# Kernel optimization log

Hardware: AMD Instinct MI355X
Metric: run time of the kernel (lower is better)

The kernel has to match this reference:

```python
import jax, jax.numpy as jnp
import numpy as np

H = 256   # rnn_hidden_size
E = 300   # embedding_size
B = 64    # batch
S = 64    # french seq len
T = 32    # max_en_length (decode steps)
VF = 32000  # french vocab
VE = 32000  # english vocab
BOS = 1


def gru_cell(x, h, wih, whh, bih, bhh):
    # torch GRUCell math: r,z,n gates, weights stored as [3H, in]/[3H, H]
    gi = x @ wih.T + bih
    gh = h @ whh.T + bhh
    ir, iz, inn = jnp.split(gi, 3, axis=-1)
    hr, hz, hn = jnp.split(gh, 3, axis=-1)
    r = jax.nn.sigmoid(ir + hr)
    z = jax.nn.sigmoid(iz + hz)
    n = jnp.tanh(inn + r * hn)
    return (1.0 - z) * n + z * h


def run_gru_dir(xs, wih, whh, bih, bhh, reverse):
    # xs: (B, S, F) -> final hidden (B, H), outputs (B, S, H) in original time order
    h0 = jnp.zeros((xs.shape[0], H), xs.dtype)
    def step(h, x):
        h2 = gru_cell(x, h, wih, whh, bih, bhh)
        return h2, h2
    hT, ys = jax.lax.scan(step, h0, jnp.swapaxes(xs, 0, 1), reverse=reverse)
    return hT, jnp.swapaxes(ys, 0, 1)


def setup_inputs() -> dict:
    key = jax.random.key(0)
    ks = iter(jax.random.split(key, 64))
    def n(shape, s=0.05):
        return jax.random.normal(next(ks), shape, dtype=jnp.float32) * s
    d = {}
    d["fr"] = jax.random.randint(next(ks), (B, S), 0, VF)
    d["fr_emb"] = n((VF, E), 0.3)
    d["en_emb"] = n((VE, E), 0.3)
    # encoder: 2 layers, bidirectional; leading dim 2 = (fwd, bwd)
    d["enc0_wih"] = n((2, 3 * H, E));      d["enc0_whh"] = n((2, 3 * H, H))
    d["enc0_bih"] = n((2, 3 * H));         d["enc0_bhh"] = n((2, 3 * H))
    d["enc1_wih"] = n((2, 3 * H, 2 * H));  d["enc1_whh"] = n((2, 3 * H, H))
    d["enc1_bih"] = n((2, 3 * H));         d["enc1_bhh"] = n((2, 3 * H))
    # decoder: 2 layers, unidirectional
    d["dec0_wih"] = n((3 * H, E));  d["dec0_whh"] = n((3 * H, H))
    d["dec0_bih"] = n((3 * H,));   d["dec0_bhh"] = n((3 * H,))
    d["dec1_wih"] = n((3 * H, H)); d["dec1_whh"] = n((3 * H, H))
    d["dec1_bih"] = n((3 * H,));   d["dec1_bhh"] = n((3 * H,))
    d["hid_w"] = n((H, 2 * H));   d["hid_b"] = n((H,))      # hidden_transformer
    d["encT_w"] = n((H, 2 * H));  d["encT_b"] = n((H,))     # encoding_transformer
    d["attn_w"] = n((H, H));      d["attn_b"] = n((H,))     # attention.hidden_linear
    d["tot_w"] = n((1, H));       d["tot_b"] = n((1,))      # attention.total_linear
    d["rnnT_w"] = n((E, 2 * H + E)); d["rnnT_b"] = n((E,))  # rnn_transformer
    d["voc_w"] = n((VE, H));      d["voc_b"] = n((VE,))     # to_vocab
    return d


def _forward(fr, fr_emb, en_emb,
             enc0_wih, enc0_whh, enc0_bih, enc0_bhh,
             enc1_wih, enc1_whh, enc1_bih, enc1_bhh,
             dec0_wih, dec0_whh, dec0_bih, dec0_bhh,
             dec1_wih, dec1_whh, dec1_bih, dec1_bhh,
             hid_w, hid_b, encT_w, encT_b, attn_w, attn_b,
             tot_w, tot_b, rnnT_w, rnnT_b, voc_w, voc_b):
    bsz = fr.shape[0]
    x = fr_emb[fr]  # (B,S,E)
    hs = []
    for (wih, whh, bih, bhh) in ((enc0_wih, enc0_whh, enc0_bih, enc0_bhh),
                                 (enc1_wih, enc1_whh, enc1_bih, enc1_bhh)):
        hf, yf = run_gru_dir(x, wih[0], whh[0], bih[0], bhh[0], reverse=False)
        hb, yb = run_gru_dir(x, wih[1], whh[1], bih[1], bhh[1], reverse=True)
        x = jnp.concatenate([yf, yb], axis=-1)  # (B,S,2H)
        hs += [hf, hb]
    encoding = x  # (B,S,2H)
    hidden = jnp.stack(hs)                       # (4,B,H) torch layout [l0f,l0b,l1f,l1b]
    hidden = hidden.reshape(2, bsz, 2 * H)       # faithful to torch .view (row-major)
    hidden = hidden @ hid_w.T + hid_b            # (2,B,H)
    trans_enc = encoding @ encT_w.T + encT_b     # (B,S,H)
    seq = en_emb[jnp.full((bsz, 1), BOS, dtype=jnp.int32)]  # (B,1,E); dropout in eval

    def dec_step(carry, _):
        hidden, seq = carry
        hq = hidden[-1][:, None, :]  # (B,1,H)
        a = jnp.tanh(trans_enc + hq @ attn_w.T + attn_b)        # (B,S,H)
        attn = jax.nn.softmax(a @ tot_w.T + tot_b, axis=1)      # (B,S,1)
        weighted = jnp.sum(attn * encoding, axis=1, keepdims=True)  # (B,1,2H)
        seq2 = jnp.concatenate([weighted, seq], axis=-1) @ rnnT_w.T + rnnT_b  # (B,1,E)
        xt = seq2[:, 0]
        h0 = gru_cell(xt, hidden[0], dec0_wih, dec0_whh, dec0_bih, dec0_bhh)
        h1 = gru_cell(h0, hidden[1], dec1_wih, dec1_whh, dec1_bih, dec1_bhh)
        logits = h1 @ voc_w.T + voc_b  # (B,VE)
        tok = jnp.argmax(logits, axis=-1)
        new_seq = en_emb[tok][:, None, :]
        return (jnp.stack([h0, h1]), new_seq), logits

    _, logits = jax.lax.scan(dec_step, (hidden, seq), None, length=T)
    return jnp.transpose(logits, (1, 0, 2))  # (B,T,VE)


def reference(fr, fr_emb, en_emb,
              enc0_wih, enc0_whh, enc0_bih, enc0_bhh,
              enc1_wih, enc1_whh, enc1_bih, enc1_bhh,
              dec0_wih, dec0_whh, dec0_bih, dec0_bhh,
              dec1_wih, dec1_whh, dec1_bih, dec1_bhh,
              hid_w, hid_b, encT_w, encT_b, attn_w, attn_b,
              tot_w, tot_b, rnnT_w, rnnT_b, voc_w, voc_b):
    return _forward(fr, fr_emb, en_emb,
                    enc0_wih, enc0_whh, enc0_bih, enc0_bhh,
                    enc1_wih, enc1_whh, enc1_bih, enc1_bhh,
                    dec0_wih, dec0_whh, dec0_bih, dec0_bhh,
                    dec1_wih, dec1_whh, dec1_bih, dec1_bhh,
                    hid_w, hid_b, encT_w, encT_b, attn_w, attn_b,
                    tot_w, tot_b, rnnT_w, rnnT_b, voc_w, voc_b)
```

## Files before the change

### kernel.cpp

```cpp
#include <hip/hip_runtime.h>
#include <math.h>

#define HD 256
#define ED 300
#define BD 64
#define SD 64
#define TD 32
#define VD 32000

__global__ void k_transpose(const float* __restrict__ in, float* __restrict__ out, int R, int K) {
    int i = blockIdx.x * 256 + threadIdx.x;
    if (i < R * K) {
        int r = i / K, k = i - r * K;
        out[(size_t)k * R + r] = in[i];
    }
}

__global__ void k_emb(const int* __restrict__ fr, const float* __restrict__ emb, float* __restrict__ x) {
    int i = blockIdx.x * 256 + threadIdx.x;
    if (i < 4096 * 300) {
        int m = i / 300, k = i - m * 300;
        int s = m >> 6, b = m & 63;
        int tok = fr[b * 64 + s];
        x[i] = emb[(size_t)tok * 300 + k];
    }
}

__launch_bounds__(256)
__global__ void k_gemm(const float* __restrict__ A, const float* __restrict__ B,
                       const float* __restrict__ bias, float* __restrict__ C,
                       int M, int N, int K) {
    __shared__ float As[16][68];
    __shared__ float Bs[16][68];
    int tid = threadIdx.x;
    int m0 = blockIdx.x * 64;
    int n0 = blockIdx.y * 64;
    int tx = tid & 15, ty = tid >> 4;
    float acc[4][4] = {};
    for (int k0 = 0; k0 < K; k0 += 16) {
        for (int e = tid; e < 1024; e += 256) {
            int mm = e >> 4, kk = e & 15;
            int k = k0 + kk;
            As[kk][mm] = (k < K) ? A[(size_t)(m0 + mm) * K + k] : 0.f;
        }
        for (int e = tid; e < 1024; e += 256) {
            int nn = e >> 4, kk = e & 15;
            int k = k0 + kk;
            Bs[kk][nn] = (k < K) ? B[(size_t)(n0 + nn) * K + k] : 0.f;
        }
        __syncthreads();
#pragma unroll
        for (int kk = 0; kk < 16; ++kk) {
            float4 a4 = *(const float4*)&As[kk][ty * 4];
            float4 b4 = *(const float4*)&Bs[kk][tx * 4];
            float av[4] = {a4.x, a4.y, a4.z, a4.w};
            float bv[4] = {b4.x, b4.y, b4.z, b4.w};
#pragma unroll
            for (int i = 0; i < 4; ++i)
#pragma unroll
                for (int j = 0; j < 4; ++j)
                    acc[i][j] += av[i] * bv[j];
        }
        __syncthreads();
    }
#pragma unroll
    for (int i = 0; i < 4; ++i) {
        int m = m0 + ty * 4 + i;
#pragma unroll
        for (int j = 0; j < 4; ++j) {
            int n = n0 + tx * 4 + j;
            C[(size_t)m * N + n] = acc[i][j] + (bias ? bias[n] : 0.f);
        }
    }
}

__launch_bounds__(512)
__global__ void k_rec(const float* __restrict__ gi, const float* __restrict__ whh_t,
                      const float* __restrict__ bhh, float* __restrict__ ys,
                      float* __restrict__ hfin) {
    __shared__ float h[2][256];
    __shared__ float part[2][3][256];
    int tid = threadIdx.x;
    int d = blockIdx.x >> 5;
    int b0 = (blockIdx.x & 31) * 2;
    h[tid >> 8][tid & 255] = 0.f;
    __syncthreads();
    int lb = 0, g = 0, qj = 0;
    bool qact = tid < 384;
    if (qact) { lb = tid / 192; int q = tid % 192; g = q >> 6; qj = q & 63; }
    const float* wp = whh_t + (size_t)d * 768 + g * 256 + qj * 4;

    for (int step = 0; step < 64; ++step) {
        int s = d ? (63 - step) : step;
        if (qact) {
            float a0 = 0.f, a1 = 0.f, a2 = 0.f, a3 = 0.f;
            const float* hp = h[lb];
#pragma unroll 4
            for (int k = 0; k < 256; ++k) {
                float4 w4 = *(const float4*)(wp + (size_t)k * 1536);
                float hk = hp[k];
                a0 += w4.x * hk; a1 += w4.y * hk; a2 += w4.z * hk; a3 += w4.w * hk;
            }
            part[lb][g][qj * 4 + 0] = a0;
            part[lb][g][qj * 4 + 1] = a1;
            part[lb][g][qj * 4 + 2] = a2;
            part[lb][g][qj * 4 + 3] = a3;
        }
        __syncthreads();
        {
            int plb = tid >> 8, j = tid & 255;
            int b = b0 + plb;
            const float* gib = gi + (size_t)(s * 64 + b) * 1536 + d * 768;
            float gr = part[plb][0][j] + bhh[d * 768 + j];
            float gz = part[plb][1][j] + bhh[d * 768 + 256 + j];
            float gn = part[plb][2][j] + bhh[d * 768 + 512 + j];
            float r = 1.f / (1.f + expf(-(gib[j] + gr)));
            float z = 1.f / (1.f + expf(-(gib[256 + j] + gz)));
            float n = tanhf(gib[512 + j] + r * gn);
            float hv = h[plb][j];
            float hn = (1.f - z) * n + z * hv;
            ys[(size_t)(s * 64 + b) * 512 + d * 256 + j] = hn;
            if (step == 63) hfin[(size_t)(d * 64 + b) * 256 + j] = hn;
            h[plb][j] = hn;
        }
        __syncthreads();
    }
}

__global__ void k_hpack(const float* __restrict__ hf0, const float* __restrict__ hf1,
                        float* __restrict__ A) {
    int i = blockIdx.x * 256 + threadIdx.x;
    if (i < 128 * 512) {
        int m = i >> 9, c = i & 511;
        int l = m >> 6, b2 = m & 63;
        int d = b2 >> 5;
        int b = 2 * (b2 & 31) + (c >> 8);
        int hh = c & 255;
        const float* src = l ? hf1 : hf0;
        A[i] = src[(size_t)(d * 64 + b) * 256 + hh];
    }
}

__launch_bounds__(256)
__global__ void k_dec1(int t,
                       const float* __restrict__ pval, const int* __restrict__ pidx,
                       const float* __restrict__ en_emb,
                       const float* __restrict__ attn_w, const float* __restrict__ attn_b,
                       const float* __restrict__ tot_w, const float* __restrict__ tot_b,
                       const float* __restrict__ te, const float* __restrict__ enc,
                       const float* __restrict__ rnnT_w, const float* __restrict__ rnnT_b,
                       const float* __restrict__ d0_wih, const float* __restrict__ d0_whh,
                       const float* __restrict__ d0_bih, const float* __restrict__ d0_bhh,
                       const float* __restrict__ d1_wih, const float* __restrict__ d1_whh,
                       const float* __restrict__ d1_bih, const float* __restrict__ d1_bhh,
                       float* __restrict__ hdec) {
    int b = blockIdx.x;
    int tid = threadIdx.x;
    __shared__ float seqv[304];
    __shared__ float hq[256];
    __shared__ float h0[256];
    __shared__ float aq[256];
    __shared__ float scred[64][4];
    __shared__ float sc[64];
    __shared__ float attnv[64];
    __shared__ float wsum[512];
    __shared__ float xt[304];
    __shared__ float h0n[256];
    __shared__ int tok_s;

    if (t == 0) {
        if (tid == 0) tok_s = 1;
    } else if (tid < 64) {
        float v = -INFINITY; int idx = 0x7fffffff;
        if (tid < 63) { v = pval[b * 64 + tid]; idx = pidx[b * 64 + tid]; }
        for (int off = 32; off > 0; off >>= 1) {
            float v2 = __shfl_down(v, off);
            int i2 = __shfl_down(idx, off);
            if (v2 > v || (v2 == v && i2 < idx)) { v = v2; idx = i2; }
        }
        if (tid == 0) tok_s = idx;
    }
    __syncthreads();
    int tok = tok_s;
    for (int e = tid; e < 300; e += 256) seqv[e] = en_emb[(size_t)tok * 300 + e];
    hq[tid] = hdec[(size_t)(64 + b) * 256 + tid];
    h0[tid] = hdec[(size_t)b * 256 + tid];
    __syncthreads();

    {
        float acc = attn_b[tid];
        const float* wr = attn_w + (size_t)tid * 256;
#pragma unroll 4
        for (int k = 0; k < 256; k += 4) {
            float4 w4 = *(const float4*)(wr + k);
            float4 h4 = *(const float4*)&hq[k];
            acc += w4.x * h4.x + w4.y * h4.y + w4.z * h4.z + w4.w * h4.w;
        }
        aq[tid] = acc;
    }
    __syncthreads();

    {
        int s = tid >> 2, p = tid & 3;
        const float* tep = te + (size_t)(s * 64 + b) * 256 + p * 64;
        float acc = 0.f;
        for (int jj = 0; jj < 64; ++jj)
            acc += tot_w[p * 64 + jj] * tanhf(tep[jj] + aq[p * 64 + jj]);
        scred[s][p] = acc;
    }
    __syncthreads();
    if (tid < 64) sc[tid] = scred[tid][0] + scred[tid][1] + scred[tid][2] + scred[tid][3] + tot_b[0];
    __syncthreads();

    if (tid < 64) {
        float v = sc[tid];
        float m = v;
        for (int off = 32; off > 0; off >>= 1) m = fmaxf(m, __shfl_xor(m, off));
        float e = expf(v - m);
        float sum = e;
        for (int off = 32; off > 0; off >>= 1) sum += __shfl_xor(sum, off);
        attnv[tid] = e / sum;
    }
    __syncthreads();

    for (int c = tid; c < 512; c += 256) {
        float acc = 0.f;
        for (int s = 0; s < 64; ++s) acc += attnv[s] * enc[(size_t)(s * 64 + b) * 512 + c];
        wsum[c] = acc;
    }
    __syncthreads();

    for (int e = tid; e < 300; e += 256) {
        float acc = rnnT_b[e];
        const float* wr = rnnT_w + (size_t)e * 812;
#pragma unroll 4
        for (int c = 0; c < 512; c += 4) {
            float4 w4 = *(const float4*)(wr + c);
            float4 s4 = *(const float4*)&wsum[c];
            acc += w4.x * s4.x + w4.y * s4.y + w4.z * s4.z + w4.w * s4.w;
        }
#pragma unroll 4
        for (int c = 0; c < 300; c += 4) {
            float4 w4 = *(const float4*)(wr + 512 + c);
            float4 s4 = *(const float4*)&seqv[c];
            acc += w4.x * s4.x + w4.y * s4.y + w4.z * s4.z + w4.w * s4.w;
        }
        xt[e] = acc;
    }
    __syncthreads();

    {
        int j = tid;
        float g0 = d0_bih[j], g1 = d0_bih[256 + j], g2 = d0_bih[512 + j];
#pragma unroll 2
        for (int k = 0; k < 300; k += 4) {
            float4 x4 = *(const float4*)&xt[k];
            float4 wa = *(const float4*)&d0_wih[(size_t)j * 300 + k];
            float4 wb = *(const float4*)&d0_wih[(size_t)(256 + j) * 300 + k];
            float4 wc = *(const float4*)&d0_wih[(size_t)(512 + j) * 300 + k];
            g0 += wa.x * x4.x + wa.y * x4.y + wa.z * x4.z + wa.w * x4.w;
            g1 += wb.x * x4.x + wb.y * x4.y + wb.z * x4.z + wb.w * x4.w;
            g2 += wc.x * x4.x + wc.y * x4.y + wc.z * x4.z + wc.w * x4.w;
        }
        float r0 = d0_bhh[j], r1 = d0_bhh[256 + j], r2 = d0_bhh[512 + j];
#pragma unroll 2
        for (int k = 0; k < 256; k += 4) {
            float4 h4 = *(const float4*)&h0[k];
            float4 wa = *(const float4*)&d0_whh[(size_t)j * 256 + k];
            float4 wb = *(const float4*)&d0_whh[(size_t)(256 + j) * 256 + k];
            float4 wc = *(const float4*)&d0_whh[(size_t)(512 + j) * 256 + k];
            r0 += wa.x * h4.x + wa.y * h4.y + wa.z * h4.z + wa.w * h4.w;
            r1 += wb.x * h4.x + wb.y * h4.y + wb.z * h4.z + wb.w * h4.w;
            r2 += wc.x * h4.x + wc.y * h4.y + wc.z * h4.z + wc.w * h4.w;
        }
        float r = 1.f / (1.f + expf(-(g0 + r0)));
        float z = 1.f / (1.f + expf(-(g1 + r1)));
        float n = tanhf(g2 + r * r2);
        float hnv = (1.f - z) * n + z * h0[j];
        hdec[(size_t)b * 256 + j] = hnv;
        h0n[j] = hnv;
    }
    __syncthreads();

    {
        int j = tid;
        float g0 = d1_bih[j], g1 = d1_bih[256 + j], g2 = d1_bih[512 + j];
#pragma unroll 2
        for (int k = 0; k < 256; k += 4) {
            float4 x4 = *(const float4*)&h0n[k];
            float4 wa = *(const float4*)&d1_wih[(size_t)j * 256 + k];
            float4 wb = *(const float4*)&d1_wih[(size_t)(256 + j) * 256 + k];
            float4 wc = *(const float4*)&d1_wih[(size_t)(512 + j) * 256 + k];
            g0 += wa.x * x4.x + wa.y * x4.y + wa.z * x4.z + wa.w * x4.w;
            g1 += wb.x * x4.x + wb.y * x4.y + wb.z * x4.z + wb.w * x4.w;
            g2 += wc.x * x4.x + wc.y * x4.y + wc.z * x4.z + wc.w * x4.w;
        }
        float r0 = d1_bhh[j], r1 = d1_bhh[256 + j], r2 = d1_bhh[512 + j];
#pragma unroll 2
        for (int k = 0; k < 256; k += 4) {
            float4 h4 = *(const float4*)&hq[k];
            float4 wa = *(const float4*)&d1_whh[(size_t)j * 256 + k];
            float4 wb = *(const float4*)&d1_whh[(size_t)(256 + j) * 256 + k];
            float4 wc = *(const float4*)&d1_whh[(size_t)(512 + j) * 256 + k];
            r0 += wa.x * h4.x + wa.y * h4.y + wa.z * h4.z + wa.w * h4.w;
            r1 += wb.x * h4.x + wb.y * h4.y + wb.z * h4.z + wb.w * h4.w;
            r2 += wc.x * h4.x + wc.y * h4.y + wc.z * h4.z + wc.w * h4.w;
        }
        float r = 1.f / (1.f + expf(-(g0 + r0)));
        float z = 1.f / (1.f + expf(-(g1 + r1)));
        float n = tanhf(g2 + r * r2);
        float hnv = (1.f - z) * n + z * hq[j];
        hdec[(size_t)(64 + b) * 256 + j] = hnv;
    }
}

__launch_bounds__(256)
__global__ void k_dec2(int t, const float* __restrict__ voc_w, const float* __restrict__ voc_b,
                       const float* __restrict__ hdec, float* __restrict__ out,
                       float* __restrict__ pval, int* __restrict__ pidx) {
    int vb = blockIdx.x, bc = blockIdx.y;
    int tid = threadIdx.x;
    int v0 = vb * 512;
    int b0 = bc * 8;
    __shared__ float hl[8][256];
    __shared__ float rv[256];
    __shared__ int ri[256];
    for (int e = tid; e < 2048; e += 256) {
        int bb = e >> 8, k = e & 255;
        hl[bb][k] = hdec[(size_t)(64 + b0 + bb) * 256 + k];
    }
    __syncthreads();
    int v1 = v0 + tid;
    int v2 = v0 + 256 + tid;
    bool has2 = v2 < VD;
    float acc1[8], acc2[8];
    float b1v = voc_b[v1];
    float b2v = has2 ? voc_b[v2] : 0.f;
#pragma unroll
    for (int bb = 0; bb < 8; ++bb) { acc1[bb] = b1v; acc2[bb] = b2v; }
    for (int k = 0; k < 256; k += 4) {
        float4 w1 = *(const float4*)&voc_w[(size_t)v1 * 256 + k];
        float4 w2 = make_float4(0.f, 0.f, 0.f, 0.f);
        if (has2) w2 = *(const float4*)&voc_w[(size_t)v2 * 256 + k];
#pragma unroll
        for (int bb = 0; bb < 8; ++bb) {
            float4 h4 = *(const float4*)&hl[bb][k];
            acc1[bb] += w1.x * h4.x + w1.y * h4.y + w1.z * h4.z + w1.w * h4.w;
            acc2[bb] += w2.x * h4.x + w2.y * h4.y + w2.z * h4.z + w2.w * h4.w;
        }
    }
    for (int bb = 0; bb < 8; ++bb) {
        int b = b0 + bb;
        out[((size_t)b * 32 + t) * VD + v1] = acc1[bb];
        if (has2) out[((size_t)b * 32 + t) * VD + v2] = acc2[bb];
        float bv = acc1[bb]; int bi = v1;
        if (has2 && (acc2[bb] > bv)) { bv = acc2[bb]; bi = v2; }
        rv[tid] = bv; ri[tid] = bi;
        __syncthreads();
        for (int stn = 128; stn > 0; stn >>= 1) {
            if (tid < stn) {
                float ov = rv[tid + stn]; int oi = ri[tid + stn];
                if (ov > rv[tid] || (ov == rv[tid] && oi < ri[tid])) { rv[tid] = ov; ri[tid] = oi; }
            }
            __syncthreads();
        }
        if (tid == 0) { pval[(size_t)b * 64 + vb] = rv[0]; pidx[(size_t)b * 64 + vb] = ri[0]; }
        __syncthreads();
    }
}

extern "C" void kernel_launch(void* const* d_in, const int* in_sizes, int n_in,
                              void* d_out, int out_size, void* d_ws, size_t ws_size,
                              hipStream_t stream) {
    (void)in_sizes; (void)n_in; (void)out_size; (void)ws_size;
    const int*   fr     = (const int*)  d_in[0];
    const float* fr_emb = (const float*)d_in[1];
    const float* en_emb = (const float*)d_in[2];
    const float* e0_wih = (const float*)d_in[3];
    const float* e0_whh = (const float*)d_in[4];
    const float* e0_bih = (const float*)d_in[5];
    const float* e0_bhh = (const float*)d_in[6];
    const float* e1_wih = (const float*)d_in[7];
    const float* e1_whh = (const float*)d_in[8];
    const float* e1_bih = (const float*)d_in[9];
    const float* e1_bhh = (const float*)d_in[10];
    const float* d0_wih = (const float*)d_in[11];
    const float* d0_whh = (const float*)d_in[12];
    const float* d0_bih = (const float*)d_in[13];
    const float* d0_bhh = (const float*)d_in[14];
    const float* d1_wih = (const float*)d_in[15];
    const float* d1_whh = (const float*)d_in[16];
    const float* d1_bih = (const float*)d_in[17];
    const float* d1_bhh = (const float*)d_in[18];
    const float* hid_w  = (const float*)d_in[19];
    const float* hid_b  = (const float*)d_in[20];
    const float* encT_w = (const float*)d_in[21];
    const float* encT_b = (const float*)d_in[22];
    const float* attn_w = (const float*)d_in[23];
    const float* attn_b = (const float*)d_in[24];
    const float* tot_w  = (const float*)d_in[25];
    const float* tot_b  = (const float*)d_in[26];
    const float* rnnT_w = (const float*)d_in[27];
    const float* rnnT_b = (const float*)d_in[28];
    const float* voc_w  = (const float*)d_in[29];
    const float* voc_b  = (const float*)d_in[30];
    float* out = (float*)d_out;

    float* ws = (float*)d_ws;
    size_t o = 0;
    auto take = [&](size_t n) { size_t r = o; o += (n + 15) & ~(size_t)15; return r; };
    float* whh0t = ws + take(256 * 1536);
    float* whh1t = ws + take(256 * 1536);
    float* xbuf  = ws + take((size_t)4096 * 300);
    float* gi    = ws + take((size_t)4096 * 1536);
    float* ys0   = ws + take((size_t)4096 * 512);
    float* ys1   = ws + take((size_t)4096 * 512);
    float* te    = ws + take((size_t)4096 * 256);
    float* hfin0 = ws + take(2 * 64 * 256);
    float* hfin1 = ws + take(2 * 64 * 256);
    float* ahid  = ws + take(128 * 512);
    float* hdec  = ws + take(128 * 256);
    float* pval  = ws + take(64 * 64);
    int*   pidx  = (int*)(ws + take(64 * 64));

    k_transpose<<<(1536 * 256 + 255) / 256, 256, 0, stream>>>(e0_whh, whh0t, 1536, 256);
    k_transpose<<<(1536 * 256 + 255) / 256, 256, 0, stream>>>(e1_whh, whh1t, 1536, 256);
    k_emb<<<(4096 * 300 + 255) / 256, 256, 0, stream>>>(fr, fr_emb, xbuf);
    k_gemm<<<dim3(64, 24), 256, 0, stream>>>(xbuf, e0_wih, e0_bih, gi, 4096, 1536, 300);
    k_rec<<<64, 512, 0, stream>>>(gi, whh0t, e0_bhh, ys0, hfin0);
    k_gemm<<<dim3(64, 24), 256, 0, stream>>>(ys0, e1_wih, e1_bih, gi, 4096, 1536, 512);
    k_rec<<<64, 512, 0, stream>>>(gi, whh1t, e1_bhh, ys1, hfin1);
    k_gemm<<<dim3(64, 4), 256, 0, stream>>>(ys1, encT_w, encT_b, te, 4096, 256, 512);
    k_hpack<<<256, 256, 0, stream>>>(hfin0, hfin1, ahid);
    k_gemm<<<dim3(2, 4), 256, 0, stream>>>(ahid, hid_w, hid_b, hdec, 128, 256, 512);
    for (int t = 0; t < 32; ++t) {
        k_dec1<<<64, 256, 0, stream>>>(t, pval, pidx, en_emb, attn_w, attn_b, tot_w, tot_b,
                                       te, ys1, rnnT_w, rnnT_b,
                                       d0_wih, d0_whh, d0_bih, d0_bhh,
                                       d1_wih, d1_whh, d1_bih, d1_bhh, hdec);
        k_dec2<<<dim3(63, 8), 256, 0, stream>>>(t, voc_w, voc_b, hdec, out, pval, pidx);
    }
}
```

Measured before the change: 12.62 ms.

## Rework GEMM tiling, recurrence, decoder and vocab projection kernels

Replaces the 64x64 GEMM with a 128x128 tile using 8x8 per-thread accumulators and float4 loads. Rewrites the encoder recurrence as one block per (direction, batch), with each thread reading its own rows of whh, which removes the transpose kernels. Widens the decoder step kernel to 1024 threads, splitting its dot products across threads with shuffle reductions. Restructures the vocab projection into 1000 blocks of 32 vocab rows covering all batches, with a transposed output staging buffer and more partial argmax entries. Workspace buffers are aliased to cut memory use, which adds reuse-ordering risk, and the larger GEMM tiles launch fewer blocks.

Result: faster. 10.94 ms (-13.3%).

```diff
diff --git a/kernel.cpp b/kernel.cpp
--- a/kernel.cpp
+++ b/kernel.cpp
@@ -1,19 +1,10 @@
 #include <hip/hip_runtime.h>
 #include <math.h>
 
-#define HD 256
-#define ED 300
-#define BD 64
-#define SD 64
-#define TD 32
 #define VD 32000
 
-__global__ void k_transpose(const float* __restrict__ in, float* __restrict__ out, int R, int K) {
-    int i = blockIdx.x * 256 + threadIdx.x;
-    if (i < R * K) {
-        int r = i / K, k = i - r * K;
-        out[(size_t)k * R + r] = in[i];
-    }
+__device__ __forceinline__ float dot4f(float4 a, float4 b) {
+    return a.x*b.x + a.y*b.y + a.z*b.z + a.w*b.w;
 }
 
 __global__ void k_emb(const int* __restrict__ fr, const float* __restrict__ emb, float* __restrict__ x) {
@@ -27,102 +18,102 @@
 }
 
 __launch_bounds__(256)
-__global__ void k_gemm(const float* __restrict__ A, const float* __restrict__ B,
-                       const float* __restrict__ bias, float* __restrict__ C,
-                       int M, int N, int K) {
-    __shared__ float As[16][68];
-    __shared__ float Bs[16][68];
+__global__ void k_gemm128(const float* __restrict__ A, const float* __restrict__ B,
+                          const float* __restrict__ bias, float* __restrict__ C,
+                          int M, int N, int K) {
+    __shared__ __align__(16) float As[16][132];
+    __shared__ __align__(16) float Bs[16][132];
     int tid = threadIdx.x;
-    int m0 = blockIdx.x * 64;
-    int n0 = blockIdx.y * 64;
+    int m0 = blockIdx.x * 128;
+    int n0 = blockIdx.y * 128;
     int tx = tid & 15, ty = tid >> 4;
-    float acc[4][4] = {};
+    float acc[8][8] = {};
     for (int k0 = 0; k0 < K; k0 += 16) {
-        for (int e = tid; e < 1024; e += 256) {
-            int mm = e >> 4, kk = e & 15;
-            int k = k0 + kk;
-            As[kk][mm] = (k < K) ? A[(size_t)(m0 + mm) * K + k] : 0.f;
-        }
-        for (int e = tid; e < 1024; e += 256) {
-            int nn = e >> 4, kk = e & 15;
-            int k = k0 + kk;
-            Bs[kk][nn] = (k < K) ? B[(size_t)(n0 + nn) * K + k] : 0.f;
+#pragma unroll
+        for (int l = 0; l < 2; ++l) {
+            int e = tid + l * 256;
+            int row = e >> 2, kc = (e & 3) << 2;
+            int k = k0 + kc;
+            float4 va = make_float4(0.f, 0.f, 0.f, 0.f);
+            float4 vb = make_float4(0.f, 0.f, 0.f, 0.f);
+            if (k < K) {
+                va = *(const float4*)&A[(size_t)(m0 + row) * K + k];
+                vb = *(const float4*)&B[(size_t)(n0 + row) * K + k];
+            }
+            As[kc + 0][row] = va.x; As[kc + 1][row] = va.y; As[kc + 2][row] = va.z; As[kc + 3][row] = va.w;
+            Bs[kc + 0][row] = vb.x; Bs[kc + 1][row] = vb.y; Bs[kc + 2][row] = vb.z; Bs[kc + 3][row] = vb.w;
         }
         __syncthreads();
 #pragma unroll
         for (int kk = 0; kk < 16; ++kk) {
-            float4 a4 = *(const float4*)&As[kk][ty * 4];
-            float4 b4 = *(const float4*)&Bs[kk][tx * 4];
-            float av[4] = {a4.x, a4.y, a4.z, a4.w};
-            float bv[4] = {b4.x, b4.y, b4.z, b4.w};
-#pragma unroll
-            for (int i = 0; i < 4; ++i)
-#pragma unroll
-                for (int j = 0; j < 4; ++j)
-                    acc[i][j] += av[i] * bv[j];
+            float a[8], bb[8];
+            *(float4*)&a[0]  = *(const float4*)&As[kk][ty * 8];
+            *(float4*)&a[4]  = *(const float4*)&As[kk][ty * 8 + 4];
+            *(float4*)&bb[0] = *(const float4*)&Bs[kk][tx * 8];
+            *(float4*)&bb[4] = *(const float4*)&Bs[kk][tx * 8 + 4];
+#pragma unroll
+            for (int i = 0; i < 8; ++i)
+#pragma unroll
+                for (int j = 0; j < 8; ++j)
+                    acc[i][j] += a[i] * bb[j];
         }
         __syncthreads();
     }
 #pragma unroll
-    for (int i = 0; i < 4; ++i) {
-        int m = m0 + ty * 4 + i;
-#pragma unroll
-        for (int j = 0; j < 4; ++j) {
-            int n = n0 + tx * 4 + j;
-            C[(size_t)m * N + n] = acc[i][j] + (bias ? bias[n] : 0.f);
-        }
-    }
-}
-
-__launch_bounds__(512)
-__global__ void k_rec(const float* __restrict__ gi, const float* __restrict__ whh_t,
+    for (int i = 0; i < 8; ++i) {
+        int m = m0 + ty * 8 + i;
+#pragma unroll
+        for (int j = 0; j < 8; j += 4) {
+            int n = n0 + tx * 8 + j;
+            float4 o;
+            o.x = acc[i][j + 0] + (bias ? bias[n + 0] : 0.f);
+            o.y = acc[i][j + 1] + (bias ? bias[n + 1] : 0.f);
+            o.z = acc[i][j + 2] + (bias ? bias[n + 2] : 0.f);
+            o.w = acc[i][j + 3] + (bias ? bias[n + 3] : 0.f);
+            *(float4*)&C[(size_t)m * N + n] = o;
+        }
+    }
+}
+
+__launch_bounds__(256)
+__global__ void k_rec(const float* __restrict__ gi, const float* __restrict__ whh,
                       const float* __restrict__ bhh, float* __restrict__ ys,
                       float* __restrict__ hfin) {
-    __shared__ float h[2][256];
-    __shared__ float part[2][3][256];
-    int tid = threadIdx.x;
-    int d = blockIdx.x >> 5;
-    int b0 = (blockIdx.x & 31) * 2;
-    h[tid >> 8][tid & 255] = 0.f;
-    __syncthreads();
-    int lb = 0, g = 0, qj = 0;
-    bool qact = tid < 384;
-    if (qact) { lb = tid / 192; int q = tid % 192; g = q >> 6; qj = q & 63; }
-    const float* wp = whh_t + (size_t)d * 768 + g * 256 + qj * 4;
-
+    __shared__ __align__(16) float h[256];
+    int u = threadIdx.x;
+    int d = blockIdx.x >> 6;
+    int b = blockIdx.x & 63;
+    h[u] = 0.f;
+    const float* wr_ = whh + ((size_t)d * 768 + u) * 256;
+    const float* wz_ = wr_ + 256 * 256;
+    const float* wn_ = wr_ + 512 * 256;
+    float br = bhh[d * 768 + u];
+    float bz = bhh[d * 768 + 256 + u];
+    float bn = bhh[d * 768 + 512 + u];
+    __syncthreads();
     for (int step = 0; step < 64; ++step) {
         int s = d ? (63 - step) : step;
-        if (qact) {
-            float a0 = 0.f, a1 = 0.f, a2 = 0.f, a3 = 0.f;
-            const float* hp = h[lb];
+        float ar = 0.f, az = 0.f, an_ = 0.f;
 #pragma unroll 4
-            for (int k = 0; k < 256; ++k) {
-                float4 w4 = *(const float4*)(wp + (size_t)k * 1536);
-                float hk = hp[k];
-                a0 += w4.x * hk; a1 += w4.y * hk; a2 += w4.z * hk; a3 += w4.w * hk;
-            }
-            part[lb][g][qj * 4 + 0] = a0;
-            part[lb][g][qj * 4 + 1] = a1;
-            part[lb][g][qj * 4 + 2] = a2;
-            part[lb][g][qj * 4 + 3] = a3;
-        }
+        for (int k = 0; k < 256; k += 4) {
+            float4 hv = *(const float4*)&h[k];
+            float4 w0 = *(const float4*)&wr_[k];
+            float4 w1 = *(const float4*)&wz_[k];
+            float4 w2 = *(const float4*)&wn_[k];
+            ar  += dot4f(w0, hv);
+            az  += dot4f(w1, hv);
+            an_ += dot4f(w2, hv);
+        }
+        const float* gib = gi + (size_t)(s * 64 + b) * 1536 + d * 768;
+        float hv_old = h[u];
+        float r = 1.f / (1.f + expf(-(gib[u] + ar + br)));
+        float z = 1.f / (1.f + expf(-(gib[256 + u] + az + bz)));
+        float n = tanhf(gib[512 + u] + r * (an_ + bn));
+        float hn = (1.f - z) * n + z * hv_old;
         __syncthreads();
-        {
-            int plb = tid >> 8, j = tid & 255;
-            int b = b0 + plb;
-            const float* gib = gi + (size_t)(s * 64 + b) * 1536 + d * 768;
-            float gr = part[plb][0][j] + bhh[d * 768 + j];
-            float gz = part[plb][1][j] + bhh[d * 768 + 256 + j];
-            float gn = part[plb][2][j] + bhh[d * 768 + 512 + j];
-            float r = 1.f / (1.f + expf(-(gib[j] + gr)));
-            float z = 1.f / (1.f + expf(-(gib[256 + j] + gz)));
-            float n = tanhf(gib[512 + j] + r * gn);
-            float hv = h[plb][j];
-            float hn = (1.f - z) * n + z * hv;
-            ys[(size_t)(s * 64 + b) * 512 + d * 256 + j] = hn;
-            if (step == 63) hfin[(size_t)(d * 64 + b) * 256 + j] = hn;
-            h[plb][j] = hn;
-        }
+        h[u] = hn;
+        ys[(size_t)(s * 64 + b) * 512 + d * 256 + u] = hn;
+        if (step == 63) hfin[(size_t)(d * 64 + b) * 256 + u] = hn;
         __syncthreads();
     }
 }
@@ -141,7 +132,7 @@
     }
 }
 
-__launch_bounds__(256)
+__launch_bounds__(1024)
 __global__ void k_dec1(int t,
                        const float* __restrict__ pval, const int* __restrict__ pidx,
                        const float* __restrict__ en_emb,
@@ -156,161 +147,169 @@
                        float* __restrict__ hdec) {
     int b = blockIdx.x;
     int tid = threadIdx.x;
-    __shared__ float seqv[304];
-    __shared__ float hq[256];
-    __shared__ float h0[256];
-    __shared__ float aq[256];
-    __shared__ float scred[64][4];
+    __shared__ __align__(16) float cat[816];
+    __shared__ __align__(16) float hq[256];
+    __shared__ __align__(16) float h0[256];
+    __shared__ __align__(16) float aq[256];
+    __shared__ __align__(16) float xt[304];
+    __shared__ __align__(16) float fpart[3][304];
+    __shared__ __align__(16) float gih[768];
+    __shared__ __align__(16) float ghh[768];
+    __shared__ __align__(16) float h0n[256];
     __shared__ float sc[64];
     __shared__ float attnv[64];
-    __shared__ float wsum[512];
-    __shared__ float xt[304];
-    __shared__ float h0n[256];
-    __shared__ int tok_s;
+    __shared__ float wv[16];
+    __shared__ int   wi[16];
+    __shared__ int   tok_s;
 
     if (t == 0) {
         if (tid == 0) tok_s = 1;
-    } else if (tid < 64) {
+    } else {
         float v = -INFINITY; int idx = 0x7fffffff;
-        if (tid < 63) { v = pval[b * 64 + tid]; idx = pidx[b * 64 + tid]; }
+        if (tid < 1000) { v = pval[(size_t)b * 1024 + tid]; idx = pidx[(size_t)b * 1024 + tid]; }
+#pragma unroll
         for (int off = 32; off > 0; off >>= 1) {
-            float v2 = __shfl_down(v, off);
-            int i2 = __shfl_down(idx, off);
+            float v2 = __shfl_down(v, off); int i2 = __shfl_down(idx, off);
             if (v2 > v || (v2 == v && i2 < idx)) { v = v2; idx = i2; }
         }
+        if ((tid & 63) == 0) { wv[tid >> 6] = v; wi[tid >> 6] = idx; }
+    }
+    __syncthreads();
+    if (t > 0 && tid < 16) {
+        float v = wv[tid]; int idx = wi[tid];
+#pragma unroll
+        for (int off = 8; off > 0; off >>= 1) {
+            float v2 = __shfl_down(v, off); int i2 = __shfl_down(idx, off);
+            if (v2 > v || (v2 == v && i2 < idx)) { v = v2; idx = i2; }
+        }
         if (tid == 0) tok_s = idx;
     }
     __syncthreads();
     int tok = tok_s;
-    for (int e = tid; e < 300; e += 256) seqv[e] = en_emb[(size_t)tok * 300 + e];
-    hq[tid] = hdec[(size_t)(64 + b) * 256 + tid];
-    h0[tid] = hdec[(size_t)b * 256 + tid];
+    if (tid < 300) cat[512 + tid] = en_emb[(size_t)tok * 300 + tid];
+    if (tid >= 512 && tid < 768) hq[tid - 512] = hdec[(size_t)(64 + b) * 256 + (tid - 512)];
+    if (tid >= 768) h0[tid - 768] = hdec[(size_t)b * 256 + (tid - 768)];
     __syncthreads();
 
     {
-        float acc = attn_b[tid];
-        const float* wr = attn_w + (size_t)tid * 256;
-#pragma unroll 4
-        for (int k = 0; k < 256; k += 4) {
-            float4 w4 = *(const float4*)(wr + k);
-            float4 h4 = *(const float4*)&hq[k];
-            acc += w4.x * h4.x + w4.y * h4.y + w4.z * h4.z + w4.w * h4.w;
-        }
-        aq[tid] = acc;
+        int j = tid >> 2, kq = tid & 3;
+        const float* wr = attn_w + (size_t)j * 256 + kq * 64;
+        const float* hp = hq + kq * 64;
+        float acc = 0.f;
+#pragma unroll
+        for (int k = 0; k < 64; k += 4)
+            acc += dot4f(*(const float4*)&wr[k], *(const float4*)&hp[k]);
+        acc += __shfl_xor(acc, 1);
+        acc += __shfl_xor(acc, 2);
+        if (kq == 0) aq[j] = acc + attn_b[j];
     }
     __syncthreads();
 
     {
-        int s = tid >> 2, p = tid & 3;
-        const float* tep = te + (size_t)(s * 64 + b) * 256 + p * 64;
+        int s = tid >> 4, p = tid & 15;
+        const float* tep = te + (size_t)(s * 64 + b) * 256 + p * 16;
+        const float* aqp = aq + p * 16;
+        const float* twp = tot_w + p * 16;
         float acc = 0.f;
-        for (int jj = 0; jj < 64; ++jj)
-            acc += tot_w[p * 64 + jj] * tanhf(tep[jj] + aq[p * 64 + jj]);
-        scred[s][p] = acc;
-    }
-    __syncthreads();
-    if (tid < 64) sc[tid] = scred[tid][0] + scred[tid][1] + scred[tid][2] + scred[tid][3] + tot_b[0];
+#pragma unroll
+        for (int jj = 0; jj < 16; ++jj)
+            acc += twp[jj] * tanhf(tep[jj] + aqp[jj]);
+#pragma unroll
+        for (int off = 8; off > 0; off >>= 1) acc += __shfl_xor(acc, off);
+        if (p == 0) sc[s] = acc + tot_b[0];
+    }
     __syncthreads();
 
     if (tid < 64) {
         float v = sc[tid];
         float m = v;
+#pragma unroll
         for (int off = 32; off > 0; off >>= 1) m = fmaxf(m, __shfl_xor(m, off));
         float e = expf(v - m);
         float sum = e;
+#pragma unroll
         for (int off = 32; off > 0; off >>= 1) sum += __shfl_xor(sum, off);
         attnv[tid] = e / sum;
     }
     __syncthreads();
 
-    for (int c = tid; c < 512; c += 256) {
+    {
+        int c = tid >> 1, sh = tid & 1;
         float acc = 0.f;
-        for (int s = 0; s < 64; ++s) acc += attnv[s] * enc[(size_t)(s * 64 + b) * 512 + c];
-        wsum[c] = acc;
-    }
-    __syncthreads();
-
-    for (int e = tid; e < 300; e += 256) {
-        float acc = rnnT_b[e];
-        const float* wr = rnnT_w + (size_t)e * 812;
+        int s0 = sh * 32;
+#pragma unroll 8
+        for (int s = s0; s < s0 + 32; ++s)
+            acc += attnv[s] * enc[(size_t)(s * 64 + b) * 512 + c];
+        acc += __shfl_xor(acc, 1);
+        if (sh == 0) cat[c] = acc;
+    }
+    __syncthreads();
+
+    if (tid < 912) {
+        int kq = tid / 304;
+        int e = tid - kq * 304;
+        if (e < 300) {
+            int k0 = kq * 272;
+            int k1 = (kq == 2) ? 812 : k0 + 272;
+            const float* wr = rnnT_w + (size_t)e * 812;
+            float acc = 0.f;
+            for (int k = k0; k < k1; k += 4)
+                acc += dot4f(*(const float4*)&wr[k], *(const float4*)&cat[k]);
+            fpart[kq][e] = acc;
+        }
+    }
+    __syncthreads();
+    if (tid < 300) xt[tid] = rnnT_b[tid] + fpart[0][tid] + fpart[1][tid] + fpart[2][tid];
+    __syncthreads();
+
+    if (tid < 768) {
+        int j = tid;
+        float gi_ = d0_bih[j];
+        const float* wi_ = d0_wih + (size_t)j * 300;
+#pragma unroll 5
+        for (int k = 0; k < 300; k += 4)
+            gi_ += dot4f(*(const float4*)&wi_[k], *(const float4*)&xt[k]);
+        float gh_ = d0_bhh[j];
+        const float* wh_ = d0_whh + (size_t)j * 256;
 #pragma unroll 4
-        for (int c = 0; c < 512; c += 4) {
-            float4 w4 = *(const float4*)(wr + c);
-            float4 s4 = *(const float4*)&wsum[c];
-            acc += w4.x * s4.x + w4.y * s4.y + w4.z * s4.z + w4.w * s4.w;
-        }
+        for (int k = 0; k < 256; k += 4)
+            gh_ += dot4f(*(const float4*)&wh_[k], *(const float4*)&h0[k]);
+        gih[j] = gi_; ghh[j] = gh_;
+    }
+    __syncthreads();
+    if (tid < 256) {
+        int u = tid;
+        float r = 1.f / (1.f + expf(-(gih[u] + ghh[u])));
+        float z = 1.f / (1.f + expf(-(gih[256 + u] + ghh[256 + u])));
+        float n = tanhf(gih[512 + u] + r * ghh[512 + u]);
+        float hv = (1.f - z) * n + z * h0[u];
+        hdec[(size_t)b * 256 + u] = hv;
+        h0n[u] = hv;
+    }
+    __syncthreads();
+
+    if (tid < 768) {
+        int j = tid;
+        float gi_ = d1_bih[j];
+        const float* wi_ = d1_wih + (size_t)j * 256;
 #pragma unroll 4
-        for (int c = 0; c < 300; c += 4) {
-            float4 w4 = *(const float4*)(wr + 512 + c);
-            float4 s4 = *(const float4*)&seqv[c];
-            acc += w4.x * s4.x + w4.y * s4.y + w4.z * s4.z + w4.w * s4.w;
-        }
-        xt[e] = acc;
-    }
-    __syncthreads();
-
-    {
-        int j = tid;
-        float g0 = d0_bih[j], g1 = d0_bih[256 + j], g2 = d0_bih[512 + j];
-#pragma unroll 2
-        for (int k = 0; k < 300; k += 4) {
-            float4 x4 = *(const float4*)&xt[k];
-            float4 wa = *(const float4*)&d0_wih[(size_t)j * 300 + k];
-            float4 wb = *(const float4*)&d0_wih[(size_t)(256 + j) * 300 + k];
-            float4 wc = *(const float4*)&d0_wih[(size_t)(512 + j) * 300 + k];
-            g0 += wa.x * x4.x + wa.y * x4.y + wa.z * x4.z + wa.w * x4.w;
-            g1 += wb.x * x4.x + wb.y * x4.y + wb.z * x4.z + wb.w * x4.w;
-            g2 += wc.x * x4.x + wc.y * x4.y + wc.z * x4.z + wc.w * x4.w;
-        }
-        float r0 = d0_bhh[j], r1 = d0_bhh[256 + j], r2 = d0_bhh[512 + j];
-#pragma unroll 2
-        for (int k = 0; k < 256; k += 4) {
-            float4 h4 = *(const float4*)&h0[k];
-            float4 wa = *(const float4*)&d0_whh[(size_t)j * 256 + k];
-            float4 wb = *(const float4*)&d0_whh[(size_t)(256 + j) * 256 + k];
-            float4 wc = *(const float4*)&d0_whh[(size_t)(512 + j) * 256 + k];
-            r0 += wa.x * h4.x + wa.y * h4.y + wa.z * h4.z + wa.w * h4.w;
-            r1 += wb.x * h4.x + wb.y * h4.y + wb.z * h4.z + wb.w * h4.w;
-            r2 += wc.x * h4.x + wc.y * h4.y + wc.z * h4.z + wc.w * h4.w;
-        }
-        float r = 1.f / (1.f + expf(-(g0 + r0)));
-        float z = 1.f / (1.f + expf(-(g1 + r1)));
-        float n = tanhf(g2 + r * r2);
-        float hnv = (1.f - z) * n + z * h0[j];
-        hdec[(size_t)b * 256 + j] = hnv;
-        h0n[j] = hnv;
-    }
-    __syncthreads();
-
-    {
-        int j = tid;
-        float g0 = d1_bih[j], g1 = d1_bih[256 + j], g2 = d1_bih[512 + j];
-#pragma unroll 2
-        for (int k = 0; k < 256; k += 4) {
-            float4 x4 = *(const float4*)&h0n[k];
-            float4 wa = *(const float4*)&d1_wih[(size_t)j * 256 + k];
-            float4 wb = *(const float4*)&d1_wih[(size_t)(256 + j) * 256 + k];
-            float4 wc = *(const float4*)&d1_wih[(size_t)(512 + j) * 256 + k];
-            g0 += wa.x * x4.x + wa.y * x4.y + wa.z * x4.z + wa.w * x4.w;
-            g1 += wb.x * x4.x + wb.y * x4.y + wb.z * x4.z + wb.w * x4.w;
-            g2 += wc.x * x4.x + wc.y * x4.y + wc.z * x4.z + wc.w * x4.w;
-        }
-        float r0 = d1_bhh[j], r1 = d1_bhh[256 + j], r2 = d1_bhh[512 + j];
-#pragma unroll 2
-        for (int k = 0; k < 256; k += 4) {
-            float4 h4 = *(const float4*)&hq[k];
-            float4 wa = *(const float4*)&d1_whh[(size_t)j * 256 + k];
-            float4 wb = *(const float4*)&d1_whh[(size_t)(256 + j) * 256 + k];
-            float4 wc = *(const float4*)&d1_whh[(size_t)(512 + j) * 256 + k];
-            r0 += wa.x * h4.x + wa.y * h4.y + wa.z * h4.z + wa.w * h4.w;
-            r1 += wb.x * h4.x + wb.y * h4.y + wb.z * h4.z + wb.w * h4.w;
-            r2 += wc.x * h4.x + wc.y * h4.y + wc.z * h4.z + wc.w * h4.w;
-        }
-        float r = 1.f / (1.f + expf(-(g0 + r0)));
-        float z = 1.f / (1.f + expf(-(g1 + r1)));
-        float n = tanhf(g2 + r * r2);
-        float hnv = (1.f - z) * n + z * hq[j];
-        hdec[(size_t)(64 + b) * 256 + j] = hnv;
+        for (int k = 0; k < 256; k += 4)
+            gi_ += dot4f(*(const float4*)&wi_[k], *(const float4*)&h0n[k]);
+        float gh_ = d1_bhh[j];
+        const float* wh_ = d1_whh + (size_t)j * 256;
+#pragma unroll 4
+        for (int k = 0; k < 256; k += 4)
+            gh_ += dot4f(*(const float4*)&wh_[k], *(const float4*)&hq[k]);
+        gih[j] = gi_; ghh[j] = gh_;
+    }
+    __syncthreads();
+    if (tid < 256) {
+        int u = tid;
+        float r = 1.f / (1.f + expf(-(gih[u] + ghh[u])));
+        float z = 1.f / (1.f + expf(-(gih[256 + u] + ghh[256 + u])));
+        float n = tanhf(gih[512 + u] + r * ghh[512 + u]);
+        float hv = (1.f - z) * n + z * hq[u];
+        hdec[(size_t)(64 + b) * 256 + u] = hv;
     }
 }
 
@@ -318,54 +317,63 @@
 __global__ void k_dec2(int t, const float* __restrict__ voc_w, const float* __restrict__ voc_b,
                        const float* __restrict__ hdec, float* __restrict__ out,
                        float* __restrict__ pval, int* __restrict__ pidx) {
-    int vb = blockIdx.x, bc = blockIdx.y;
+    __shared__ float hlT[256 * 66];
+    __shared__ float outT[32 * 66];
+    __shared__ float pm_v[4 * 64];
+    __shared__ int   pm_i[4 * 64];
     int tid = threadIdx.x;
-    int v0 = vb * 512;
-    int b0 = bc * 8;
-    __shared__ float hl[8][256];
-    __shared__ float rv[256];
-    __shared__ int ri[256];
+    int bx = blockIdx.x;
+    int v0 = bx * 32;
+    int w = tid >> 6, lb = tid & 63;
+
+    for (int e = tid; e < 4096; e += 256) {
+        int bb = e >> 6, kq = (e & 63) << 2;
+        float4 hv = *(const float4*)&hdec[(size_t)(64 + bb) * 256 + kq];
+        hlT[(kq + 0) * 66 + bb] = hv.x;
+        hlT[(kq + 1) * 66 + bb] = hv.y;
+        hlT[(kq + 2) * 66 + bb] = hv.z;
+        hlT[(kq + 3) * 66 + bb] = hv.w;
+    }
+    __syncthreads();
+
+    const float* wbase = voc_w + (size_t)(v0 + w * 8) * 256;
+    float acc[8];
+#pragma unroll
+    for (int r = 0; r < 8; ++r) acc[r] = voc_b[v0 + w * 8 + r];
+    for (int k = 0; k < 256; k += 4) {
+        float h0_ = hlT[(k + 0) * 66 + lb];
+        float h1_ = hlT[(k + 1) * 66 + lb];
+        float h2_ = hlT[(k + 2) * 66 + lb];
+        float h3_ = hlT[(k + 3) * 66 + lb];
+#pragma unroll
+        for (int r = 0; r < 8; ++r) {
+            float4 w4 = *(const float4*)&wbase[(size_t)r * 256 + k];
+            acc[r] += w4.x * h0_ + w4.y * h1_ + w4.z * h2_ + w4.w * h3_;
+        }
+    }
+    float bv = acc[0]; int bi = v0 + w * 8;
+#pragma unroll
+    for (int r = 1; r < 8; ++r)
+        if (acc[r] > bv) { bv = acc[r]; bi = v0 + w * 8 + r; }
+#pragma unroll
+    for (int r = 0; r < 8; ++r) outT[(w * 8 + r) * 66 + lb] = acc[r];
+    pm_v[w * 64 + lb] = bv;
+    pm_i[w * 64 + lb] = bi;
+    __syncthreads();
+
     for (int e = tid; e < 2048; e += 256) {
-        int bb = e >> 8, k = e & 255;
-        hl[bb][k] = hdec[(size_t)(64 + b0 + bb) * 256 + k];
-    }
-    __syncthreads();
-    int v1 = v0 + tid;
-    int v2 = v0 + 256 + tid;
-    bool has2 = v2 < VD;
-    float acc1[8], acc2[8];
-    float b1v = voc_b[v1];
-    float b2v = has2 ? voc_b[v2] : 0.f;
-#pragma unroll
-    for (int bb = 0; bb < 8; ++bb) { acc1[bb] = b1v; acc2[bb] = b2v; }
-    for (int k = 0; k < 256; k += 4) {
-        float4 w1 = *(const float4*)&voc_w[(size_t)v1 * 256 + k];
-        float4 w2 = make_float4(0.f, 0.f, 0.f, 0.f);
-        if (has2) w2 = *(const float4*)&voc_w[(size_t)v2 * 256 + k];
-#pragma unroll
-        for (int bb = 0; bb < 8; ++bb) {
-            float4 h4 = *(const float4*)&hl[bb][k];
-            acc1[bb] += w1.x * h4.x + w1.y * h4.y + w1.z * h4.z + w1.w * h4.w;
-            acc2[bb] += w2.x * h4.x + w2.y * h4.y + w2.z * h4.z + w2.w * h4.w;
-        }
-    }
-    for (int bb = 0; bb < 8; ++bb) {
-        int b = b0 + bb;
-        out[((size_t)b * 32 + t) * VD + v1] = acc1[bb];
-        if (has2) out[((size_t)b * 32 + t) * VD + v2] = acc2[bb];
-        float bv = acc1[bb]; int bi = v1;
-        if (has2 && (acc2[bb] > bv)) { bv = acc2[bb]; bi = v2; }
-        rv[tid] = bv; ri[tid] = bi;
-        __syncthreads();
-        for (int stn = 128; stn > 0; stn >>= 1) {
-            if (tid < stn) {
-                float ov = rv[tid + stn]; int oi = ri[tid + stn];
-                if (ov > rv[tid] || (ov == rv[tid] && oi < ri[tid])) { rv[tid] = ov; ri[tid] = oi; }
-            }
-            __syncthreads();
-        }
-        if (tid == 0) { pval[(size_t)b * 64 + vb] = rv[0]; pidx[(size_t)b * 64 + vb] = ri[0]; }
-        __syncthreads();
+        int bb = e >> 5, vl = e & 31;
+        out[((size_t)bb * 32 + t) * VD + v0 + vl] = outT[vl * 66 + bb];
+    }
+    if (tid < 64) {
+        float v = pm_v[tid]; int idx = pm_i[tid];
+#pragma unroll
+        for (int ww = 1; ww < 4; ++ww) {
+            float ov = pm_v[ww * 64 + tid]; int oi = pm_i[ww * 64 + tid];
+            if (ov > v || (ov == v && oi < idx)) { v = ov; idx = oi; }
+        }
+        pval[(size_t)tid * 1024 + bx] = v;
+        pidx[(size_t)tid * 1024 + bx] = idx;
     }
 }
 
@@ -409,35 +417,32 @@
     float* ws = (float*)d_ws;
     size_t o = 0;
     auto take = [&](size_t n) { size_t r = o; o += (n + 15) & ~(size_t)15; return r; };
-    float* whh0t = ws + take(256 * 1536);
-    float* whh1t = ws + take(256 * 1536);
-    float* xbuf  = ws + take((size_t)4096 * 300);
+    float* ys0   = ws + take((size_t)4096 * 512);
     float* gi    = ws + take((size_t)4096 * 1536);
-    float* ys0   = ws + take((size_t)4096 * 512);
     float* ys1   = ws + take((size_t)4096 * 512);
-    float* te    = ws + take((size_t)4096 * 256);
     float* hfin0 = ws + take(2 * 64 * 256);
     float* hfin1 = ws + take(2 * 64 * 256);
-    float* ahid  = ws + take(128 * 512);
-    float* hdec  = ws + take(128 * 256);
-    float* pval  = ws + take(64 * 64);
-    int*   pidx  = (int*)(ws + take(64 * 64));
-
-    k_transpose<<<(1536 * 256 + 255) / 256, 256, 0, stream>>>(e0_whh, whh0t, 1536, 256);
-    k_transpose<<<(1536 * 256 + 255) / 256, 256, 0, stream>>>(e1_whh, whh1t, 1536, 256);
+
+    float* xbuf = ys0;
+    float* te   = gi;
+    float* ahid = gi + (size_t)4096 * 256;
+    float* hdec = ahid + 128 * 512;
+    float* pval = hdec + 128 * 256;
+    int*   pidx = (int*)(pval + 64 * 1024);
+
     k_emb<<<(4096 * 300 + 255) / 256, 256, 0, stream>>>(fr, fr_emb, xbuf);
-    k_gemm<<<dim3(64, 24), 256, 0, stream>>>(xbuf, e0_wih, e0_bih, gi, 4096, 1536, 300);
-    k_rec<<<64, 512, 0, stream>>>(gi, whh0t, e0_bhh, ys0, hfin0);
-    k_gemm<<<dim3(64, 24), 256, 0, stream>>>(ys0, e1_wih, e1_bih, gi, 4096, 1536, 512);
-    k_rec<<<64, 512, 0, stream>>>(gi, whh1t, e1_bhh, ys1, hfin1);
-    k_gemm<<<dim3(64, 4), 256, 0, stream>>>(ys1, encT_w, encT_b, te, 4096, 256, 512);
+    k_gemm128<<<dim3(32, 12), 256, 0, stream>>>(xbuf, e0_wih, e0_bih, gi, 4096, 1536, 300);
+    k_rec<<<128, 256, 0, stream>>>(gi, e0_whh, e0_bhh, ys0, hfin0);
+    k_gemm128<<<dim3(32, 12), 256, 0, stream>>>(ys0, e1_wih, e1_bih, gi, 4096, 1536, 512);
+    k_rec<<<128, 256, 0, stream>>>(gi, e1_whh, e1_bhh, ys1, hfin1);
+    k_gemm128<<<dim3(32, 2), 256, 0, stream>>>(ys1, encT_w, encT_b, te, 4096, 256, 512);
     k_hpack<<<256, 256, 0, stream>>>(hfin0, hfin1, ahid);
-    k_gemm<<<dim3(2, 4), 256, 0, stream>>>(ahid, hid_w, hid_b, hdec, 128, 256, 512);
+    k_gemm128<<<dim3(1, 2), 256, 0, stream>>>(ahid, hid_w, hid_b, hdec, 128, 256, 512);
     for (int t = 0; t < 32; ++t) {
-        k_dec1<<<64, 256, 0, stream>>>(t, pval, pidx, en_emb, attn_w, attn_b, tot_w, tot_b,
-                                       te, ys1, rnnT_w, rnnT_b,
-                                       d0_wih, d0_whh, d0_bih, d0_bhh,
-                                       d1_wih, d1_whh, d1_bih, d1_bhh, hdec);
-        k_dec2<<<dim3(63, 8), 256, 0, stream>>>(t, voc_w, voc_b, hdec, out, pval, pidx);
-    }
-}
+        k_dec1<<<64, 1024, 0, stream>>>(t, pval, pidx, en_emb, attn_w, attn_b, tot_w, tot_b,
+                                        te, ys1, rnnT_w, rnnT_b,
+                                        d0_wih, d0_whh, d0_bih, d0_bhh,
+                                        d1_wih, d1_whh, d1_bih, d1_bhh, hdec);
+        k_dec2<<<1000, 256, 0, stream>>>(t, voc_w, voc_b, hdec, out, pval, pidx);
+    }
+}
```
